# Kernel optimization log

Hardware: AMD Instinct MI355X
Metric: run time of the kernel (lower is better)

Reference implementation:

```python
import math
import jax, jax.numpy as jnp
import numpy as np

EPS = 1e-05
_THETA = 180.0 * math.pi / 180.0
COS_T = math.cos(_THETA)   # -1.0
SIN_T = math.sin(_THETA)   # ~1.22e-16 (kept for faithfulness)
FH, FW = 3, 3
SH, SW = 1, 1
PH, PW = 1, 1


def _unfold(x):
    # x: (N, C, H, W) -> patches (N, C*FH*FW, OH, OW), channel-major (c, fh, fw)
    # ordering, matching torch.nn.functional.unfold.
    return jax.lax.conv_general_dilated_patches(
        x, (FH, FW), (SH, SW), [(PH, PH), (PW, PW)])


def _norm(v, axis=-1):
    return jnp.sqrt(jnp.sum(v * v, axis=axis, keepdims=True))


def m_rule(w, x, r, eps):
    # w: (n_filters, in_dim), x: (bs, in_dim), r: (bs, n_filters)
    normalized_w = w / (_norm(w) + eps)                       # (nf, d)
    norm_x = _norm(x) + eps                                   # (bs, 1)
    normalized_x = x / norm_x                                 # (bs, d)
    wx = normalized_x @ normalized_w.T                        # (bs, nf)
    # orth = w_hat - (w_hat . x_hat) x_hat, per (patch, filter) pair
    orth = normalized_w[None, :, :] - wx[:, :, None] * normalized_x[:, None, :]
    normalized_orth = orth / (_norm(orth) + eps)              # (bs, nf, d)
    x_head = (COS_T * normalized_x[:, None, :] + SIN_T * normalized_orth)
    x_head = x_head * norm_x[:, :, None]                      # (bs, nf, d)
    x_diff = x[:, None, :] - x_head                           # (bs, nf, d)
    wx_diff = w[None, :, :] * x_diff                          # (bs, nf, d)
    wx_diff_normalized = wx_diff / (wx_diff.sum(-1, keepdims=True) + eps)
    r_out = wx_diff_normalized * r[:, :, None]                # (bs, nf, d)
    return r_out.sum(1)                                       # (bs, d)


def setup_inputs() -> dict:
    key = jax.random.key(0)
    k1, k2, k3 = jax.random.split(key, 3)
    x = jax.random.normal(k1, (4, 64, 16, 16), dtype=jnp.float32)
    r = jax.random.normal(k2, (4, 128, 16, 16), dtype=jnp.float32)
    weight = jax.random.normal(k3, (128, 64, 3, 3), dtype=jnp.float32) * 0.05
    return {"x": x, "r": r, "weight": weight}


def reference(x, r, weight):
    N, C, H, W = x.shape
    NF = weight.shape[0]
    patches = _unfold(x)                                      # (N, C*9, OH, OW)
    _, IN_DIM, OH, OW = patches.shape
    x_col = patches.reshape(N, IN_DIM, OH * OW).transpose(0, 2, 1).reshape(-1, IN_DIM)
    w_col = weight.reshape(NF, -1)                            # (NF, C*9)
    r_col = r.transpose(0, 2, 3, 1).reshape(-1, NF)           # (N*OH*OW, NF)
    r_new = m_rule(w_col, x_col, r_col, EPS)                  # (N*OH*OW, C*9)
    r_img = r_new.reshape(N, OH * OW, IN_DIM).transpose(0, 2, 1).reshape(N, IN_DIM, OH, OW)
    # F.fold is the linear transpose (adjoint) of unfold: overlapping patches
    # are summed back into the (N, C, H, W) image.
    fold = jax.linear_transpose(_unfold, jax.ShapeDtypeStruct(x.shape, x.dtype))
    return fold(r_img)[0]
```

## Files before the change

### kernel.cpp

```cpp
#include <hip/hip_runtime.h>

constexpr int N  = 4, C = 64, H = 16, W = 16;
constexpr int NF = 128;
constexpr int D  = C * 9;
constexpr float EPSF = 1e-5f;

__global__ void k_prep(const float* __restrict__ w,
                       float* __restrict__ w_t, float* __restrict__ w2f) {
    int gid = blockIdx.x * blockDim.x + threadIdx.x;
    if (gid < D * NF) {
        int k = gid / NF, f = gid % NF;
        w_t[gid] = w[f * D + k];
    } else {
        int g = gid - D * NF;
        if (g < NF * 9 * C) {
            int c = g % C;
            int t = g / C;
            int ab = t % 9, f = t / 9;
            int a = ab / 3, b = ab % 3;
            w2f[g] = w[f * D + c * 9 + (2 - a) * 3 + (2 - b)];
        }
    }
}

__global__ void __launch_bounds__(512) k_conv_t(
        const float* __restrict__ x, const float* __restrict__ w_t,
        const float* __restrict__ r, float* __restrict__ t_g) {
    __shared__ double part[3][NF][4];

    const int bid = blockIdx.x;
    const int ow0 = (bid & 3) * 4;
    const int oh  = (bid >> 2) & 15;
    const int n   = bid >> 6;
    const int tid = threadIdx.x;
    const int f   = tid & 127;
    const int cg  = tid >> 7;
    const int iw0 = ow0 - 1;

    double a0 = 0, a1 = 0, a2 = 0, a3 = 0;
    const float* __restrict__ wp = w_t + f;

    for (int ci = 0; ci < 16; ++ci) {
        const int c = cg * 16 + ci;
        const float* xbase = x + ((n * C + c) * H) * W;
#pragma unroll
        for (int dh = 0; dh < 3; ++dh) {
            const int ih = oh - 1 + dh;
            float xr[6];
            if (ih >= 0 && ih < H) {
                const float* xrow = xbase + ih * W;
#pragma unroll
                for (int j = 0; j < 6; ++j) {
                    int iw = iw0 + j;
                    xr[j] = (iw >= 0 && iw < W) ? xrow[iw] : 0.f;
                }
            } else {
#pragma unroll
                for (int j = 0; j < 6; ++j) xr[j] = 0.f;
            }
            double xd[6];
#pragma unroll
            for (int j = 0; j < 6; ++j) xd[j] = (double)xr[j];
            const int kbase = (c * 9 + dh * 3) * NF;
#pragma unroll
            for (int b = 0; b < 3; ++b) {
                double wd = (double)wp[kbase + b * NF];
                a0 += wd * xd[b];
                a1 += wd * xd[b + 1];
                a2 += wd * xd[b + 2];
                a3 += wd * xd[b + 3];
            }
        }
    }

    if (cg > 0) {
        part[cg - 1][f][0] = a0; part[cg - 1][f][1] = a1;
        part[cg - 1][f][2] = a2; part[cg - 1][f][3] = a3;
    }
    __syncthreads();
    if (cg == 0) {
#pragma unroll
        for (int g = 0; g < 3; ++g) {
            a0 += part[g][f][0]; a1 += part[g][f][1];
            a2 += part[g][f][2]; a3 += part[g][f][3];
        }
        const int base = ((n * NF + f) * H + oh) * W + ow0;
        const float* rp = r + base;
        float* tp = t_g + base;
        tp[0] = (float)((2.0 * (double)rp[0]) / (2.0 * a0 + (double)EPSF));
        tp[1] = (float)((2.0 * (double)rp[1]) / (2.0 * a1 + (double)EPSF));
        tp[2] = (float)((2.0 * (double)rp[2]) / (2.0 * a2 + (double)EPSF));
        tp[3] = (float)((2.0 * (double)rp[3]) / (2.0 * a3 + (double)EPSF));
    }
}

__global__ void __launch_bounds__(512) k_convT_out(
        const float* __restrict__ x, const float* __restrict__ w2f,
        const float* __restrict__ t_g, float* __restrict__ out) {
    __shared__ float part[7][C][4];

    const int bid = blockIdx.x;
    const int w0  = (bid & 3) * 4;
    const int h   = (bid >> 2) & 15;
    const int n   = bid >> 6;
    const int tid = threadIdx.x;
    const int c   = tid & 63;
    const int fg  = tid >> 6;
    const int iw0 = w0 - 1;

    float a0 = 0, a1 = 0, a2 = 0, a3 = 0;

    for (int fi = 0; fi < 16; ++fi) {
        const int f = fg * 16 + fi;
        const float* tbase = t_g + ((n * NF + f) * H) * W;
        const float* __restrict__ wfa = w2f + (f * 9) * C + c;
#pragma unroll
        for (int a = 0; a < 3; ++a) {
            const int oh2 = h - 1 + a;
            float tr[6];
            if (oh2 >= 0 && oh2 < H) {
                const float* trow = tbase + oh2 * W;
#pragma unroll
                for (int j = 0; j < 6; ++j) {
                    int ow = iw0 + j;
                    tr[j] = (ow >= 0 && ow < W) ? trow[ow] : 0.f;
                }
            } else {
#pragma unroll
                for (int j = 0; j < 6; ++j) tr[j] = 0.f;
            }
#pragma unroll
            for (int b = 0; b < 3; ++b) {
                float wv = wfa[(a * 3 + b) * C];
                a0 += wv * tr[b];
                a1 += wv * tr[b + 1];
                a2 += wv * tr[b + 2];
                a3 += wv * tr[b + 3];
            }
        }
    }

    if (fg > 0) {
        part[fg - 1][c][0] = a0; part[fg - 1][c][1] = a1;
        part[fg - 1][c][2] = a2; part[fg - 1][c][3] = a3;
    }
    __syncthreads();
    if (fg == 0) {
#pragma unroll
        for (int g = 0; g < 7; ++g) {
            a0 += part[g][c][0]; a1 += part[g][c][1];
            a2 += part[g][c][2]; a3 += part[g][c][3];
        }
        const int base = ((n * C + c) * H + h) * W + w0;
        out[base + 0] = x[base + 0] * a0;
        out[base + 1] = x[base + 1] * a1;
        out[base + 2] = x[base + 2] * a2;
        out[base + 3] = x[base + 3] * a3;
    }
}

extern "C" void kernel_launch(void* const* d_in, const int* in_sizes, int n_in,
                              void* d_out, int out_size, void* d_ws, size_t ws_size,
                              hipStream_t stream) {
    const float* x = (const float*)d_in[0];
    const float* r = (const float*)d_in[1];
    const float* w = (const float*)d_in[2];
    float* out = (float*)d_out;

    float* ws   = (float*)d_ws;
    float* w_t  = ws;
    float* w2f  = w_t + D * NF;
    float* t_g  = w2f + NF * 9 * C;

    k_prep<<<(2 * D * NF + 255) / 256, 256, 0, stream>>>(w, w_t, w2f);
    k_conv_t<<<256, 512, 0, stream>>>(x, w_t, r, t_g);
    k_convT_out<<<256, 512, 0, stream>>>(x, w2f, t_g, out);
}
```

Baseline: 85.99 us.

## Fuse three kernels into one cooperative kernel with grid syncs and 1024 threads

Replaces the weight-prep, conv and transposed-conv kernels with one cooperative kernel that separates the stages with grid-wide syncs. Block size doubles to 1024 threads, so each thread handles half as many channels or filters and the shared-memory partial reductions grow to 8 and 16 groups. The aim is to remove two kernel launch gaps and add parallelism per block. In exchange it pays for grid.sync, needs all 256 blocks of 1024 threads co-resident, and does a longer serial reduction in shared memory.

```diff
diff --git a/kernel.cpp b/kernel.cpp
--- a/kernel.cpp
+++ b/kernel.cpp
@@ -1,161 +1,170 @@
 #include <hip/hip_runtime.h>
+#include <hip/hip_cooperative_groups.h>
+
+namespace cg = cooperative_groups;
 
 constexpr int N  = 4, C = 64, H = 16, W = 16;
 constexpr int NF = 128;
 constexpr int D  = C * 9;
 constexpr float EPSF = 1e-5f;
 
-__global__ void k_prep(const float* __restrict__ w,
-                       float* __restrict__ w_t, float* __restrict__ w2f) {
-    int gid = blockIdx.x * blockDim.x + threadIdx.x;
-    if (gid < D * NF) {
-        int k = gid / NF, f = gid % NF;
-        w_t[gid] = w[f * D + k];
-    } else {
-        int g = gid - D * NF;
-        if (g < NF * 9 * C) {
-            int c = g % C;
-            int t = g / C;
-            int ab = t % 9, f = t / 9;
-            int a = ab / 3, b = ab % 3;
-            w2f[g] = w[f * D + c * 9 + (2 - a) * 3 + (2 - b)];
+__global__ void __launch_bounds__(1024) k_fused(
+        const float* __restrict__ x, const float* __restrict__ r,
+        const float* __restrict__ w, float* __restrict__ out,
+        float* __restrict__ w_t, float* __restrict__ w2f,
+        float* __restrict__ t_g) {
+    __shared__ double partd[4 * 7 * 128];
+    cg::grid_group grid = cg::this_grid();
+    const int bid = blockIdx.x;
+    const int tid = threadIdx.x;
+
+    {
+        const int base = bid * 288;
+        for (int i = tid; i < 288; i += 1024) {
+            const int g = base + i;
+            const int k = g / NF, f = g % NF;
+            w_t[g] = w[f * D + k];
+            const int c2 = g % C;
+            const int t2 = g / C;
+            const int ab = t2 % 9, f2 = t2 / 9;
+            const int a = ab / 3, b = ab % 3;
+            w2f[g] = w[f2 * D + c2 * 9 + (2 - a) * 3 + (2 - b)];
         }
     }
-}
+    grid.sync();
 
-__global__ void __launch_bounds__(512) k_conv_t(
-        const float* __restrict__ x, const float* __restrict__ w_t,
-        const float* __restrict__ r, float* __restrict__ t_g) {
-    __shared__ double part[3][NF][4];
+    {
+        const int ow0 = (bid & 3) * 4;
+        const int oh  = (bid >> 2) & 15;
+        const int n   = bid >> 6;
+        const int f   = tid & 127;
+        const int cgi = tid >> 7;
+        const int iw0 = ow0 - 1;
 
-    const int bid = blockIdx.x;
-    const int ow0 = (bid & 3) * 4;
-    const int oh  = (bid >> 2) & 15;
-    const int n   = bid >> 6;
-    const int tid = threadIdx.x;
-    const int f   = tid & 127;
-    const int cg  = tid >> 7;
-    const int iw0 = ow0 - 1;
+        double a0 = 0, a1 = 0, a2 = 0, a3 = 0;
+        const float* __restrict__ wp = w_t + f;
 
-    double a0 = 0, a1 = 0, a2 = 0, a3 = 0;
-    const float* __restrict__ wp = w_t + f;
-
-    for (int ci = 0; ci < 16; ++ci) {
-        const int c = cg * 16 + ci;
-        const float* xbase = x + ((n * C + c) * H) * W;
+        for (int ci = 0; ci < 8; ++ci) {
+            const int c = cgi * 8 + ci;
+            const float* xbase = x + ((n * C + c) * H) * W;
 #pragma unroll
-        for (int dh = 0; dh < 3; ++dh) {
-            const int ih = oh - 1 + dh;
-            float xr[6];
-            if (ih >= 0 && ih < H) {
-                const float* xrow = xbase + ih * W;
+            for (int dh = 0; dh < 3; ++dh) {
+                const int ih = oh - 1 + dh;
+                float xr[6];
+                if (ih >= 0 && ih < H) {
+                    const float* xrow = xbase + ih * W;
 #pragma unroll
-                for (int j = 0; j < 6; ++j) {
-                    int iw = iw0 + j;
-                    xr[j] = (iw >= 0 && iw < W) ? xrow[iw] : 0.f;
+                    for (int j = 0; j < 6; ++j) {
+                        const int iw = iw0 + j;
+                        xr[j] = (iw >= 0 && iw < W) ? xrow[iw] : 0.f;
+                    }
+                } else {
+#pragma unroll
+                    for (int j = 0; j < 6; ++j) xr[j] = 0.f;
                 }
-            } else {
+                double xd[6];
 #pragma unroll
-                for (int j = 0; j < 6; ++j) xr[j] = 0.f;
-            }
-            double xd[6];
+                for (int j = 0; j < 6; ++j) xd[j] = (double)xr[j];
+                const int kbase = (c * 9 + dh * 3) * NF;
 #pragma unroll
-            for (int j = 0; j < 6; ++j) xd[j] = (double)xr[j];
-            const int kbase = (c * 9 + dh * 3) * NF;
-#pragma unroll
-            for (int b = 0; b < 3; ++b) {
-                double wd = (double)wp[kbase + b * NF];
-                a0 += wd * xd[b];
-                a1 += wd * xd[b + 1];
-                a2 += wd * xd[b + 2];
-                a3 += wd * xd[b + 3];
+                for (int b = 0; b < 3; ++b) {
+                    const double wd = (double)wp[kbase + b * NF];
+                    a0 += wd * xd[b];
+                    a1 += wd * xd[b + 1];
+                    a2 += wd * xd[b + 2];
+                    a3 += wd * xd[b + 3];
+                }
             }
         }
+
+        if (cgi > 0) {
+            partd[(0 * 7 + cgi - 1) * 128 + f] = a0;
+            partd[(1 * 7 + cgi - 1) * 128 + f] = a1;
+            partd[(2 * 7 + cgi - 1) * 128 + f] = a2;
+            partd[(3 * 7 + cgi - 1) * 128 + f] = a3;
+        }
+        __syncthreads();
+        if (cgi == 0) {
+#pragma unroll
+            for (int g = 0; g < 7; ++g) {
+                a0 += partd[(0 * 7 + g) * 128 + f];
+                a1 += partd[(1 * 7 + g) * 128 + f];
+                a2 += partd[(2 * 7 + g) * 128 + f];
+                a3 += partd[(3 * 7 + g) * 128 + f];
+            }
+            const int base = ((n * NF + f) * H + oh) * W + ow0;
+            const float* rp = r + base;
+            float* tp = t_g + base;
+            tp[0] = (float)((2.0 * (double)rp[0]) / (2.0 * a0 + (double)EPSF));
+            tp[1] = (float)((2.0 * (double)rp[1]) / (2.0 * a1 + (double)EPSF));
+            tp[2] = (float)((2.0 * (double)rp[2]) / (2.0 * a2 + (double)EPSF));
+            tp[3] = (float)((2.0 * (double)rp[3]) / (2.0 * a3 + (double)EPSF));
+        }
     }
+    grid.sync();
 
-    if (cg > 0) {
-        part[cg - 1][f][0] = a0; part[cg - 1][f][1] = a1;
-        part[cg - 1][f][2] = a2; part[cg - 1][f][3] = a3;
-    }
-    __syncthreads();
-    if (cg == 0) {
+    {
+        const int w0 = (bid & 3) * 4;
+        const int h  = (bid >> 2) & 15;
+        const int n  = bid >> 6;
+        const int c  = tid & 63;
+        const int fg = tid >> 6;
+        const int iw0 = w0 - 1;
+
+        float b0 = 0, b1 = 0, b2 = 0, b3 = 0;
+
+        for (int fi = 0; fi < 8; ++fi) {
+            const int f = fg * 8 + fi;
+            const float* tbase = t_g + ((n * NF + f) * H) * W;
+            const float* __restrict__ wfa = w2f + (f * 9) * C + c;
 #pragma unroll
-        for (int g = 0; g < 3; ++g) {
-            a0 += part[g][f][0]; a1 += part[g][f][1];
-            a2 += part[g][f][2]; a3 += part[g][f][3];
-        }
-        const int base = ((n * NF + f) * H + oh) * W + ow0;
-        const float* rp = r + base;
-        float* tp = t_g + base;
-        tp[0] = (float)((2.0 * (double)rp[0]) / (2.0 * a0 + (double)EPSF));
-        tp[1] = (float)((2.0 * (double)rp[1]) / (2.0 * a1 + (double)EPSF));
-        tp[2] = (float)((2.0 * (double)rp[2]) / (2.0 * a2 + (double)EPSF));
-        tp[3] = (float)((2.0 * (double)rp[3]) / (2.0 * a3 + (double)EPSF));
-    }
-}
-
-__global__ void __launch_bounds__(512) k_convT_out(
-        const float* __restrict__ x, const float* __restrict__ w2f,
-        const float* __restrict__ t_g, float* __restrict__ out) {
-    __shared__ float part[7][C][4];
-
-    const int bid = blockIdx.x;
-    const int w0  = (bid & 3) * 4;
-    const int h   = (bid >> 2) & 15;
-    const int n   = bid >> 6;
-    const int tid = threadIdx.x;
-    const int c   = tid & 63;
-    const int fg  = tid >> 6;
-    const int iw0 = w0 - 1;
-
-    float a0 = 0, a1 = 0, a2 = 0, a3 = 0;
-
-    for (int fi = 0; fi < 16; ++fi) {
-        const int f = fg * 16 + fi;
-        const float* tbase = t_g + ((n * NF + f) * H) * W;
-        const float* __restrict__ wfa = w2f + (f * 9) * C + c;
+            for (int a = 0; a < 3; ++a) {
+                const int oh2 = h - 1 + a;
+                float tr[6];
+                if (oh2 >= 0 && oh2 < H) {
+                    const float* trow = tbase + oh2 * W;
 #pragma unroll
-        for (int a = 0; a < 3; ++a) {
-            const int oh2 = h - 1 + a;
-            float tr[6];
-            if (oh2 >= 0 && oh2 < H) {
-                const float* trow = tbase + oh2 * W;
+                    for (int j = 0; j < 6; ++j) {
+                        const int ow = iw0 + j;
+                        tr[j] = (ow >= 0 && ow < W) ? trow[ow] : 0.f;
+                    }
+                } else {
 #pragma unroll
-                for (int j = 0; j < 6; ++j) {
-                    int ow = iw0 + j;
-                    tr[j] = (ow >= 0 && ow < W) ? trow[ow] : 0.f;
+                    for (int j = 0; j < 6; ++j) tr[j] = 0.f;
                 }
-            } else {
 #pragma unroll
-                for (int j = 0; j < 6; ++j) tr[j] = 0.f;
-            }
-#pragma unroll
-            for (int b = 0; b < 3; ++b) {
-                float wv = wfa[(a * 3 + b) * C];
-                a0 += wv * tr[b];
-                a1 += wv * tr[b + 1];
-                a2 += wv * tr[b + 2];
-                a3 += wv * tr[b + 3];
+                for (int b = 0; b < 3; ++b) {
+                    const float wv = wfa[(a * 3 + b) * C];
+                    b0 += wv * tr[b];
+                    b1 += wv * tr[b + 1];
+                    b2 += wv * tr[b + 2];
+                    b3 += wv * tr[b + 3];
+                }
             }
         }
-    }
 
-    if (fg > 0) {
-        part[fg - 1][c][0] = a0; part[fg - 1][c][1] = a1;
-        part[fg - 1][c][2] = a2; part[fg - 1][c][3] = a3;
-    }
-    __syncthreads();
-    if (fg == 0) {
+        float* fpart = (float*)partd;
+        if (fg > 0) {
+            fpart[(0 * 15 + fg - 1) * 64 + c] = b0;
+            fpart[(1 * 15 + fg - 1) * 64 + c] = b1;
+            fpart[(2 * 15 + fg - 1) * 64 + c] = b2;
+            fpart[(3 * 15 + fg - 1) * 64 + c] = b3;
+        }
+        __syncthreads();
+        if (fg == 0) {
 #pragma unroll
-        for (int g = 0; g < 7; ++g) {
-            a0 += part[g][c][0]; a1 += part[g][c][1];
-            a2 += part[g][c][2]; a3 += part[g][c][3];
+            for (int g = 0; g < 15; ++g) {
+                b0 += fpart[(0 * 15 + g) * 64 + c];
+                b1 += fpart[(1 * 15 + g) * 64 + c];
+                b2 += fpart[(2 * 15 + g) * 64 + c];
+                b3 += fpart[(3 * 15 + g) * 64 + c];
+            }
+            const int base = ((n * C + c) * H + h) * W + w0;
+            out[base + 0] = x[base + 0] * b0;
+            out[base + 1] = x[base + 1] * b1;
+            out[base + 2] = x[base + 2] * b2;
+            out[base + 3] = x[base + 3] * b3;
         }
-        const int base = ((n * C + c) * H + h) * W + w0;
-        out[base + 0] = x[base + 0] * a0;
-        out[base + 1] = x[base + 1] * a1;
-        out[base + 2] = x[base + 2] * a2;
-        out[base + 3] = x[base + 3] * a3;
     }
 }
 
@@ -172,7 +181,8 @@
     float* w2f  = w_t + D * NF;
     float* t_g  = w2f + NF * 9 * C;
 
-    k_prep<<<(2 * D * NF + 255) / 256, 256, 0, stream>>>(w, w_t, w2f);
-    k_conv_t<<<256, 512, 0, stream>>>(x, w_t, r, t_g);
-    k_convT_out<<<256, 512, 0, stream>>>(x, w2f, t_g, out);
+    void* args[] = {(void*)&x, (void*)&r, (void*)&w, (void*)&out,
+                    (void*)&w_t, (void*)&w2f, (void*)&t_g};
+    hipLaunchCooperativeKernel((const void*)k_fused, dim3(256), dim3(1024),
+                               args, 0, stream);
 }
```

Measured after the change: 146.6 us. 70.4% more time.
